# Performance work log

Measured on AMD Instinct MI355X. Metric: run time of the kernel, lower is better.

Reference implementation:

```python
import jax, jax.numpy as jnp
import numpy as np
import math

HIDDEN = 1024
NUM_HEADS = 16
HEAD_DIM = HIDDEN // NUM_HEADS
B, S = 4, 1024


def setup_inputs() -> dict:
    key = jax.random.key(0)
    ks = jax.random.split(key, 16)
    sd = 1.0 / math.sqrt(HIDDEN)
    inp = {
        "x": jax.random.normal(ks[0], (B, S, HIDDEN), jnp.float32),
        "spikes": jax.random.uniform(ks[1], (B, S, HIDDEN), jnp.float32),
        "membrane_potential": jax.random.normal(ks[2], (B, S, HIDDEN), jnp.float32),
        "Wq": jax.random.normal(ks[3], (HIDDEN, HIDDEN), jnp.float32) * sd,
        "bq": jnp.zeros((HIDDEN,), jnp.float32),
        "Wk": jax.random.normal(ks[4], (HIDDEN, HIDDEN), jnp.float32) * sd,
        "bk": jnp.zeros((HIDDEN,), jnp.float32),
        "Wv": jax.random.normal(ks[5], (HIDDEN, HIDDEN), jnp.float32) * sd,
        "bv": jnp.zeros((HIDDEN,), jnp.float32),
        "Wo": jax.random.normal(ks[6], (HIDDEN, HIDDEN), jnp.float32) * sd,
        "bo": jnp.zeros((HIDDEN,), jnp.float32),
        "tau_decay": jnp.ones((NUM_HEADS,), jnp.float32) * 10.0,
        "Wg": jax.random.normal(ks[7], (HIDDEN, 2 * HIDDEN), jnp.float32) * sd,
        "bg": jnp.zeros((HIDDEN,), jnp.float32),
    }
    return inp


def _heads(t):  # [B,S,H] -> [B,nH,S,hd]
    Bv, Sv, _ = t.shape
    return t.reshape(Bv, Sv, NUM_HEADS, HEAD_DIM).transpose(0, 2, 1, 3)


def reference(x, spikes, membrane_potential, Wq, bq, Wk, bk, Wv, bv, Wo, bo, tau_decay, Wg, bg):
    scale = 1.0 / math.sqrt(HEAD_DIM)
    q = _heads(x @ Wq.T + bq)
    k = _heads(x @ Wk.T + bk)
    v = _heads(x @ Wv.T + bv)

    # raw scores [B,nH,S,S]
    scores = jnp.einsum('bhqd,bhkd->bhqk', q, k) * scale

    # per-head exponential temporal decay mask [nH,S,S]
    times = jnp.arange(S, dtype=jnp.float32)
    tdiff = jnp.abs(times[:, None] - times[None, :])  # [S,S]
    tmask = jnp.exp(-tdiff[None] / tau_decay[:, None, None])
    scores = scores * tmask[None]

    # spike correlation term
    sm = _heads(spikes)
    spike_attn = jnp.einsum('bhqd,bhkd->bhqk', sm, sm) * scale
    scores = scores * (1.0 + spike_attn)

    # membrane gating of V
    v = v * jax.nn.sigmoid(_heads(membrane_potential))

    probs = jax.nn.softmax(scores, axis=-1)
    context = jnp.einsum('bhqk,bhkd->bhqd', probs, v)
    context = context.transpose(0, 2, 1, 3).reshape(B, S, HIDDEN)

    # dendritic gate
    gate_in = jnp.concatenate([context, membrane_potential], axis=-1)
    gate = jax.nn.sigmoid(gate_in @ Wg.T + bg)
    context = context * gate

    return context @ Wo.T + bo
```

## Files before the change

### kernel.cpp

```cpp
#include <hip/hip_runtime.h>
#include <math.h>
#include <stdint.h>

namespace {

typedef __attribute__((ext_vector_type(8))) short s8v;
typedef __attribute__((ext_vector_type(4))) float f4v;
typedef unsigned short u16;

__device__ __forceinline__ float fexp2(float x) {
  return __builtin_amdgcn_exp2f(x);
}

__device__ __forceinline__ u16 f2bf(float f) {
  union { float f; uint32_t u; } v; v.f = f;
  uint32_t r = v.u + 0x7fffu + ((v.u >> 16) & 1u);
  return (u16)(r >> 16);
}
__device__ __forceinline__ float bf2f(u16 h) {
  union { uint32_t u; float f; } v; v.u = ((uint32_t)h) << 16;
  return v.f;
}
__device__ __forceinline__ uint32_t pk2r(float a, float b) {
  return (uint32_t)f2bf(a) | ((uint32_t)f2bf(b) << 16);
}
__device__ __forceinline__ uint32_t pk2(float a, float b) {
  union { float f; uint32_t u; } x, y; x.f = a; y.f = b;
  return ((x.u + 0x8000u) >> 16) | ((y.u + 0x8000u) & 0xffff0000u);
}
__device__ __forceinline__ float sigmoidf_(float x) { return 1.0f / (1.0f + __expf(-x)); }

__device__ __forceinline__ void gload16(const u16* g, u16* l) {
  __builtin_amdgcn_global_load_lds(
      (const __attribute__((address_space(1))) void*)g,
      (__attribute__((address_space(3))) void*)l, 16, 0, 0);
}

struct CvtJob { const float* src; u16* dst; };
struct CvtArgs { CvtJob j[18]; float* vz; };

__global__ __launch_bounds__(256) void cvt_kernel(CvtArgs a) {
  if (blockIdx.y == 0 && blockIdx.x < 4) {
    float4 z; z.x = 0.f; z.y = 0.f; z.z = 0.f; z.w = 0.f;
    ((float4*)a.vz)[blockIdx.x * 256 + threadIdx.x] = z;
  }
  const CvtJob jb = a.j[blockIdx.y];
  const int i = blockIdx.x * 256 + threadIdx.x;
  const float4 v = ((const float4*)jb.src)[i];
  uint2 pk;
  pk.x = pk2r(v.x, v.y);
  pk.y = pk2r(v.z, v.w);
  ((uint2*)jb.dst)[i] = pk;
}

__global__ __launch_bounds__(768, 3) void qkv_gemm(
    const u16* __restrict__ xb,
    const u16* __restrict__ Wqb, const u16* __restrict__ Wkb, const u16* __restrict__ Wvb,
    const float* __restrict__ bq, const float* __restrict__ bk, const float* __restrict__ bv,
    const u16* __restrict__ memb,
    u16* __restrict__ Qb, u16* __restrict__ Kb, u16* __restrict__ Vt,
    float* __restrict__ Vtot) {
  __shared__ __align__(16) u16 as_[4][4096];
  __shared__ __align__(16) u16 bs_[4][12288];
  const int t = threadIdx.x;
  const int nb = blockIdx.x, mb = blockIdx.y;
  const int m0 = mb * 128, n0 = nb * 128;
  const int l = t & 63, w = t >> 6;
  const int mat = w >> 2;
  const int wl = w & 3, wm = wl >> 1, wn = wl & 1;
  const int lr = l & 15, lq = l >> 4;
  const int rh = lr >> 1;
  const int rb4 = (lr & 1) << 2;
  const int bmat = mat * 4096;

  const f4v fz = {0.f, 0.f, 0.f, 0.f};
  f4v acc[4][4];
#pragma unroll
  for (int i = 0; i < 4; ++i)
#pragma unroll
    for (int j = 0; j < 4; ++j) acc[i][j] = fz;

  const int tt = t & 255, uu = (t >> 8) & 1;
  const int sc0 = (tt & 7) ^ ((tt >> 3) & 7);
  const int sgrow = ((tt >> 3) << 1) + (sc0 >> 2);
  const int sgk = (sc0 & 3) << 3;
  const bool stg = (t < 512);

  const u16* ga = xb + (size_t)(m0 + uu * 64 + sgrow) * 1024 + sgk;
  const u16* gq = Wqb + (size_t)(n0 + uu * 64 + sgrow) * 1024 + sgk;
  const u16* gk = Wkb + (size_t)(n0 + uu * 64 + sgrow) * 1024 + sgk;
  const u16* gv = Wvb + (size_t)(n0 + uu * 64 + sgrow) * 1024 + sgk;
  const int lofs = uu * 2048 + tt * 8;

#define QKV_STAGE(c)                                                           \
  {                                                                            \
    const int ko_ = (c) * 32;                                                  \
    const int bb_ = (c) & 3;                                                   \
    gload16(ga + ko_, &as_[bb_][lofs]);                                        \
    gload16(gq + ko_, &bs_[bb_][lofs]);                                        \
    gload16(gk + ko_, &bs_[bb_][4096 + lofs]);                                 \
    gload16(gv + ko_, &bs_[bb_][8192 + lofs]);                                 \
  }

  if (stg) { QKV_STAGE(0); QKV_STAGE(1); QKV_STAGE(2); }
  asm volatile("s_waitcnt vmcnt(8)" ::: "memory");
  __builtin_amdgcn_s_barrier();

  const int co = ((rb4 + lq) ^ rh) * 8;
  for (int c = 0; c < 32; ++c) {
    const int cb = c & 3;
    const bool st = (c + 3 < 32);
    s8v af[4], bf[4];
#pragma unroll
    for (int mi = 0; mi < 4; ++mi)
      af[mi] = *(const s8v*)(&as_[cb][(wm * 32 + mi * 8 + rh) * 64 + co]);
#pragma unroll
    for (int ni = 0; ni < 4; ++ni)
      bf[ni] = *(const s8v*)(&bs_[cb][bmat + (wn * 32 + ni * 8 + rh) * 64 + co]);
    if (stg && st) QKV_STAGE(c + 3);
    __builtin_amdgcn_s_barrier();
    asm volatile("s_waitcnt lgkmcnt(0)" ::: "memory");
    __builtin_amdgcn_sched_barrier(0);
    __builtin_amdgcn_s_setprio(1);
    if (mat < 2) {
#pragma unroll
      for (int mi = 0; mi < 4; ++mi)
#pragma unroll
        for (int ni = 0; ni < 4; ++ni)
          acc[mi][ni] = __builtin_amdgcn_mfma_f32_16x16x32_bf16(
              bf[ni], af[mi], acc[mi][ni], 0, 0, 0);
    } else {
#pragma unroll
      for (int mi = 0; mi < 4; ++mi)
#pragma unroll
        for (int ni = 0; ni < 4; ++ni)
          acc[mi][ni] = __builtin_amdgcn_mfma_f32_16x16x32_bf16(
              af[mi], bf[ni], acc[mi][ni], 0, 0, 0);
    }
    __builtin_amdgcn_s_setprio(0);
    if (st) {
      asm volatile("s_waitcnt vmcnt(8)" ::: "memory");
    } else if (c == 29) {
      asm volatile("s_waitcnt vmcnt(4)" ::: "memory");
    } else if (c == 30) {
      asm volatile("s_waitcnt vmcnt(0)" ::: "memory");
    }
    if (c < 31) __builtin_amdgcn_s_barrier();
  }
#undef QKV_STAGE
  __builtin_amdgcn_sched_barrier(0);

  if (mat < 2) {
    u16* dst = (mat == 0) ? Qb : Kb;
    const float* bias = (mat == 0) ? bq : bk;
#pragma unroll
    for (int mi = 0; mi < 4; ++mi)
#pragma unroll
      for (int ni = 0; ni < 4; ++ni) {
        const int m = m0 + wm * 64 + mi * 16 + lr;
        const int nb4 = n0 + wn * 64 + ni * 16 + lq * 4;
        const float4 b4 = *(const float4*)&bias[nb4];
        uint2 pk;
        pk.x = pk2r(acc[mi][ni][0] + b4.x, acc[mi][ni][1] + b4.y);
        pk.y = pk2r(acc[mi][ni][2] + b4.z, acc[mi][ni][3] + b4.w);
        *(uint2*)(dst + (size_t)m * 1024 + nb4) = pk;
      }
  } else {
    const int b = m0 >> 10;
    float vpart[4] = {0.f, 0.f, 0.f, 0.f};
#pragma unroll
    for (int mi = 0; mi < 4; ++mi)
#pragma unroll
      for (int ni = 0; ni < 4; ++ni) {
        const int mrow = m0 + wm * 64 + mi * 16 + lq * 4;
        const int ncol = n0 + wn * 64 + ni * 16 + lr;
        const int h = ncol >> 6, d = ncol & 63;
        const float bi = bv[ncol];
        float tv[4];
#pragma unroll
        for (int r = 0; r < 4; ++r)
          tv[r] = (acc[mi][ni][r] + bi) *
                  sigmoidf_(bf2f(memb[(size_t)(mrow + r) * 1024 + ncol]));
        vpart[ni] += (tv[0] + tv[1]) + (tv[2] + tv[3]);
        const int s = mrow & 1023;
        uint2 pk;
        pk.x = pk2r(tv[0], tv[1]);
        pk.y = pk2r(tv[2], tv[3]);
        *(uint2*)(Vt + ((size_t)((b * 16 + h) * 64 + d)) * 1024 + s) = pk;
      }
#pragma unroll
    for (int ni = 0; ni < 4; ++ni) {
      const int ncol = n0 + wn * 64 + ni * 16 + lr;
      atomicAdd(&Vtot[(size_t)(b * 16 + (ncol >> 6)) * 64 + (ncol & 63)], vpart[ni]);
    }
  }
}

template <int MODE>
__global__ __launch_bounds__(512, 2) void gemm64(
    const u16* __restrict__ Ab, const u16* __restrict__ A2b,
    const u16* __restrict__ W, const float* __restrict__ bias,
    u16* __restrict__ outb, float* __restrict__ outf, int K) {
  __shared__ __align__(16) u16 as_[4][4096], bs_[4][4096];
  const int t = threadIdx.x;
  const int m0 = blockIdx.y * 128, n0 = blockIdx.x * 128;
  const int l = t & 63, w = t >> 6;
  const int wm = w >> 2, wn = w & 3;
  const int lr = l & 15, lq = l >> 4;
  const int rh = lr >> 1, rb4 = (lr & 1) << 2;
  const f4v fz = {0.f, 0.f, 0.f, 0.f};
  f4v acc[4][2];
#pragma unroll
  for (int i = 0; i < 4; ++i)
#pragma unroll
    for (int j = 0; j < 2; ++j) acc[i][j] = fz;

  const int tt = t & 255, uu = t >> 8;
  const int sc0 = (tt & 7) ^ ((tt >> 3) & 7);
  const int sgrow = ((tt >> 3) << 1) + (sc0 >> 2);
  const int sgk = (sc0 & 3) << 3;
  const u16* ga1 = Ab + (size_t)(m0 + uu * 64 + sgrow) * 1024 + sgk;
  const u16* ga2 = (MODE == 1)
      ? (A2b + (size_t)(m0 + uu * 64 + sgrow) * 1024 + sgk) : ga1;
  const u16* gw = W + (size_t)(n0 + uu * 64 + sgrow) * K + sgk;
  const int lofs = uu * 2048 + tt * 8;
  const int nc = K >> 5;

#define G_STAGE_A(c)                                                           \
  {                                                                            \
    const int ko_ = (c) * 32;                                                  \
    if (MODE == 1 && ko_ >= 1024) gload16(ga2 + (ko_ - 1024), &as_[(c) & 3][lofs]); \
    else gload16(ga1 + ko_, &as_[(c) & 3][lofs]);                              \
  }
#define G_STAGE_W(c) gload16(gw + (c) * 32, &bs_[(c) & 3][lofs])

  G_STAGE_A(0); G_STAGE_W(0);
  G_STAGE_A(1); G_STAGE_W(1);
  G_STAGE_A(2); G_STAGE_W(2);
  asm volatile("s_waitcnt vmcnt(4)" ::: "memory");
  __builtin_amdgcn_s_barrier();

  const int co = ((rb4 + lq) ^ rh) * 8;
  for (int c = 0; c < nc; ++c) {
    const int cb = c & 3;
    s8v af[4], bf[2];
#pragma unroll
    for (int mi = 0; mi < 4; ++mi)
      af[mi] = *(const s8v*)(&as_[cb][(wm * 32 + mi * 8 + rh) * 64 + co]);
#pragma unroll
    for (int ni = 0; ni < 2; ++ni)
      bf[ni] = *(const s8v*)(&bs_[cb][(wn * 16 + ni * 8 + rh) * 64 + co]);
    if (c + 3 < nc) { G_STAGE_A(c + 3); G_STAGE_W(c + 3); }
    __builtin_amdgcn_s_barrier();
    asm volatile("s_waitcnt lgkmcnt(0)" ::: "memory");
    __builtin_amdgcn_sched_barrier(0);
    __builtin_amdgcn_s_setprio(1);
#pragma unroll
    for (int mi = 0; mi < 4; ++mi)
#pragma unroll
      for (int ni = 0; ni < 2; ++ni)
        acc[mi][ni] = __builtin_amdgcn_mfma_f32_16x16x32_bf16(
            bf[ni], af[mi], acc[mi][ni], 0, 0, 0);
    __builtin_amdgcn_s_setprio(0);
    if (c + 3 < nc) {
      asm volatile("s_waitcnt vmcnt(4)" ::: "memory");
    } else if (c + 3 == nc) {
      asm volatile("s_waitcnt vmcnt(2)" ::: "memory");
    } else if (c + 2 == nc) {
      asm volatile("s_waitcnt vmcnt(0)" ::: "memory");
    }
    if (c + 1 < nc) __builtin_amdgcn_s_barrier();
  }
#undef G_STAGE_A
#undef G_STAGE_W
  __builtin_amdgcn_sched_barrier(0);

#pragma unroll
  for (int mi = 0; mi < 4; ++mi)
#pragma unroll
    for (int ni = 0; ni < 2; ++ni) {
      const int m = m0 + wm * 64 + mi * 16 + lr;
      const int nb4 = n0 + wn * 32 + ni * 16 + lq * 4;
      const float4 b4 = *(const float4*)&bias[nb4];
      if (MODE == 0) {
        float4 o;
        o.x = acc[mi][ni][0] + b4.x; o.y = acc[mi][ni][1] + b4.y;
        o.z = acc[mi][ni][2] + b4.z; o.w = acc[mi][ni][3] + b4.w;
        *(float4*)(outf + (size_t)m * 1024 + nb4) = o;
      } else {
        const uint2 a2 = *(const uint2*)(Ab + (size_t)m * 1024 + nb4);
        float cx[4] = {bf2f((u16)(a2.x & 0xffff)), bf2f((u16)(a2.x >> 16)),
                       bf2f((u16)(a2.y & 0xffff)), bf2f((u16)(a2.y >> 16))};
        float g[4];
        g[0] = cx[0] * sigmoidf_(acc[mi][ni][0] + b4.x);
        g[1] = cx[1] * sigmoidf_(acc[mi][ni][1] + b4.y);
        g[2] = cx[2] * sigmoidf_(acc[mi][ni][2] + b4.z);
        g[3] = cx[3] * sigmoidf_(acc[mi][ni][3] + b4.w);
        uint2 pk;
        pk.x = pk2r(g[0], g[1]);
        pk.y = pk2r(g[2], g[3]);
        *(uint2*)(outb + (size_t)m * 1024 + nb4) = pk;
      }
    }
}

__global__ __launch_bounds__(256) void attn_mfma(
    const u16* __restrict__ Qb, const u16* __restrict__ Kb,
    const u16* __restrict__ SPb, const u16* __restrict__ Vt,
    const float* __restrict__ tau, const float* __restrict__ Vtot,
    u16* __restrict__ CTXb) {
  __shared__ u16 kbuf[4096], skbuf[4096], vbuf[4096];
  __shared__ u16 pbuf[4][16 * 64];
  const int t = threadIdx.x, l = t & 63, w = t >> 6;
  const int lr = l & 15, lq = l >> 4;
  const int p = blockIdx.x;
  const int g = (p & 7) + 8 * (p >> 7);
  const int qt = (p >> 3) & 15;
  const int h = g & 15, b = g >> 4;

  const float tv_ = tau[h];
  const float c2 = 1.44269504088896f / tv_;
  const float K0 = 0.125f * 1.44269504088896f;
  int rad = (int)ceilf(tv_ * 0.171875f);
  if (rad > 15) rad = 15;
  const int jlo = (qt - rad < 0) ? 0 : qt - rad;
  const int jhi = (qt + rad > 15) ? 15 : qt + rad;
  const int farCnt = 16 - (jhi - jlo + 1);

  float cN[4], cNi[4], cR[4], cRi[4];
#pragma unroll
  for (int i = 0; i < 4; ++i) {
    cN[i]  = fexp2(c2 * (float)(i * 16));
    cNi[i] = fexp2(-c2 * (float)(i * 16));
    cR[i]  = fexp2(c2 * (float)(lq * 4 + i));
    cRi[i] = fexp2(-c2 * (float)(lq * 4 + i));
  }

  s8v qf[2], sf[2];
  {
    const size_t base = ((size_t)(b * 1024 + qt * 64 + w * 16 + lr)) * 1024 + h * 64 + lq * 8;
    qf[0] = *(const s8v*)(Qb + base);
    qf[1] = *(const s8v*)(Qb + base + 32);
    sf[0] = *(const s8v*)(SPb + base);
    sf[1] = *(const s8v*)(SPb + base + 32);
  }
  const s8v ones = {0x3F80, 0x3F80, 0x3F80, 0x3F80, 0x3F80, 0x3F80, 0x3F80, 0x3F80};

  const f4v fz = {0.f, 0.f, 0.f, 0.f};
  f4v oacc[4], vs[4];
  float lacc[4];
#pragma unroll
  for (int i = 0; i < 4; ++i) { oacc[i] = fz; vs[i] = fz; lacc[i] = 0.f; }

  const int iqw = qt * 64 + w * 16;
  const int srow = t >> 3;
  const int csw = ((t & 7) ^ (srow & 7)) * 8;
  const int rx = lr & 7;
  u16* pw = pbuf[w];

  for (int jc = jlo; jc <= jhi; ++jc) {
    const int j0 = jc * 64;
    __syncthreads();
    {
      const size_t kg = ((size_t)(b * 1024 + j0 + srow)) * 1024 + h * 64 + csw;
      gload16(Kb + kg, kbuf + t * 8);
      gload16(Kb + kg + 32 * 1024, kbuf + 2048 + t * 8);
      gload16(SPb + kg, skbuf + t * 8);
      gload16(SPb + kg + 32 * 1024, skbuf + 2048 + t * 8);
      const size_t vg = ((size_t)((b * 16 + h) * 64 + srow)) * 1024 + j0 + csw;
      gload16(Vt + vg, vbuf + t * 8);
      gload16(Vt + vg + 32 * 1024, vbuf + 2048 + t * 8);
    }
    __syncthreads();

    f4v sa[4], ssa[4];
#pragma unroll
    for (int ni = 0; ni < 4; ++ni) { sa[ni] = fz; ssa[ni] = fz; }
#pragma unroll
    for (int ks = 0; ks < 2; ++ks) {
#pragma unroll
      for (int ni = 0; ni < 4; ++ni) {
        const int off = (ni * 16 + lr) * 64 + (((ks * 4 + lq) ^ rx) * 8);
        const s8v kf = *(const s8v*)(kbuf + off);
        sa[ni] = __builtin_amdgcn_mfma_f32_16x16x32_bf16(kf, qf[ks], sa[ni], 0, 0, 0);
        const s8v skf = *(const s8v*)(skbuf + off);
        ssa[ni] = __builtin_amdgcn_mfma_f32_16x16x32_bf16(skf, sf[ks], ssa[ni], 0, 0, 0);
      }
    }

    const int D0 = iqw - j0;
    float pv[4][4];
    if (jc < qt) {
      const float EA = K0 * fexp2(-c2 * (float)(D0 + lr));
#pragma unroll
      for (int ni = 0; ni < 4; ++ni)
#pragma unroll
        for (int r = 0; r < 4; ++r) {
          const float t1 = fmaf(ssa[ni][r], 0.125f, 1.0f);
          const float e = fexp2(sa[ni][r] * cN[ni] * cR[r] * EA * t1);
          pv[ni][r] = e;
          lacc[ni] += e;
        }
    } else if (jc > qt) {
      const float EAi = K0 * fexp2(c2 * (float)(D0 + lr));
#pragma unroll
      for (int ni = 0; ni < 4; ++ni)
#pragma unroll
        for (int r = 0; r < 4; ++r) {
          const float t1 = fmaf(ssa[ni][r], 0.125f, 1.0f);
          const float e = fexp2(sa[ni][r] * cNi[ni] * cRi[r] * EAi * t1);
          pv[ni][r] = e;
          lacc[ni] += e;
        }
    } else {
      const float EA  = K0 * fexp2(-c2 * (float)(D0 + lr));
      const float EAi = K0 * fexp2(c2 * (float)(D0 + lr));
#pragma unroll
      for (int ni = 0; ni < 4; ++ni)
#pragma unroll
        for (int r = 0; r < 4; ++r) {
          const int jloc = ni * 16 + lq * 4 + r;
          const float fb = cN[ni] * cR[r] * EA;
          const float fa = cNi[ni] * cRi[r] * EAi;
          const float f = (D0 + lr >= jloc) ? fb : fa;
          const float t1 = fmaf(ssa[ni][r], 0.125f, 1.0f);
          const float e = fexp2(sa[ni][r] * f * t1);
          pv[ni][r] = e;
          lacc[ni] += e;
        }
    }

#pragma unroll
    for (int ni = 0; ni < 4; ++ni) {
      const int phys = (ni * 2 + (lq >> 1)) ^ rx;
      uint2 p2;
      p2.x = pk2(pv[ni][0], pv[ni][1]);
      p2.y = pk2(pv[ni][2], pv[ni][3]);
      *(uint2*)(pw + lr * 64 + phys * 8 + (lq & 1) * 4) = p2;
    }

#pragma unroll
    for (int ks = 0; ks < 2; ++ks) {
      const s8v pf = *(const s8v*)(pw + lr * 64 + (((ks * 4 + lq) ^ rx) * 8));
#pragma unroll
      for (int nd = 0; nd < 4; ++nd) {
        const int off = (nd * 16 + lr) * 64 + (((ks * 4 + lq) ^ rx) * 8);
        const s8v vf = *(const s8v*)(vbuf + off);
        oacc[nd] = __builtin_amdgcn_mfma_f32_16x16x32_bf16(vf, pf, oacc[nd], 0, 0, 0);
        vs[nd] = __builtin_amdgcn_mfma_f32_16x16x32_bf16(vf, ones, vs[nd], 0, 0, 0);
      }
    }
  }

  float ls = (lacc[0] + lacc[1]) + (lacc[2] + lacc[3]);
  ls += __shfl_xor(ls, 16);
  ls += __shfl_xor(ls, 32);
  ls += 64.0f * (float)farCnt;
  const float inv = 1.0f / ls;
  const float* vt0 = Vtot + (size_t)(b * 16 + h) * 64;
  const size_t orow = ((size_t)(b * 1024 + qt * 64 + w * 16 + lr)) * 1024 + h * 64;
#pragma unroll
  for (int nd = 0; nd < 4; ++nd) {
    const float4 vt4 = *(const float4*)(vt0 + nd * 16 + lq * 4);
    float o0 = (oacc[nd][0] + vt4.x - vs[nd][0]) * inv;
    float o1 = (oacc[nd][1] + vt4.y - vs[nd][1]) * inv;
    float o2 = (oacc[nd][2] + vt4.z - vs[nd][2]) * inv;
    float o3 = (oacc[nd][3] + vt4.w - vs[nd][3]) * inv;
    uint2 o;
    o.x = pk2r(o0, o1);
    o.y = pk2r(o2, o3);
    *(uint2*)(CTXb + orow + nd * 16 + lq * 4) = o;
  }
}

}

extern "C" void kernel_launch(void* const* d_in, const int* in_sizes, int n_in,
                              void* d_out, int out_size, void* d_ws, size_t ws_size,
                              hipStream_t stream) {
  const float* x      = (const float*)d_in[0];
  const float* spikes = (const float*)d_in[1];
  const float* mem    = (const float*)d_in[2];
  const float* Wq     = (const float*)d_in[3];
  const float* bq     = (const float*)d_in[4];
  const float* Wk     = (const float*)d_in[5];
  const float* bk     = (const float*)d_in[6];
  const float* Wv     = (const float*)d_in[7];
  const float* bv     = (const float*)d_in[8];
  const float* Wo     = (const float*)d_in[9];
  const float* bo     = (const float*)d_in[10];
  const float* tau    = (const float*)d_in[11];
  const float* Wg     = (const float*)d_in[12];
  const float* bg     = (const float*)d_in[13];
  float* out = (float*)d_out;

  uint8_t* w8 = (uint8_t*)d_ws;
  u16* spb  = (u16*)(w8);
  u16* xb   = (u16*)(w8 + (8u << 20));
  u16* Wqb  = (u16*)(w8 + (16u << 20));
  u16* Wkb  = (u16*)(w8 + (18u << 20));
  u16* Wvb  = (u16*)(w8 + (20u << 20));
  u16* Wob  = (u16*)(w8 + (22u << 20));
  u16* Wgb  = (u16*)(w8 + (24u << 20));
  u16* Qb   = (u16*)(w8 + (28u << 20));
  u16* Kb   = (u16*)(w8 + (36u << 20));
  u16* Vt   = (u16*)(w8 + (44u << 20));
  u16* CTXb = (u16*)(w8 + (52u << 20));
  float* Vtot = (float*)(w8 + (60u << 20));
  u16* memb = (u16*)d_out;
  u16* gctx = xb;

  constexpr size_t QE = 262144 * 4;
  CvtArgs ca;
  for (int q = 0; q < 4; ++q) ca.j[q]     = {x + q * QE,      xb + q * QE};
  for (int q = 0; q < 4; ++q) ca.j[4 + q] = {spikes + q * QE, spb + q * QE};
  for (int q = 0; q < 4; ++q) ca.j[8 + q] = {mem + q * QE,    memb + q * QE};
  ca.j[12] = {Wq, Wqb};
  ca.j[13] = {Wk, Wkb};
  ca.j[14] = {Wv, Wvb};
  ca.j[15] = {Wo, Wob};
  ca.j[16] = {Wg, Wgb};
  ca.j[17] = {Wg + QE, Wgb + QE};
  ca.vz = Vtot;
  cvt_kernel<<<dim3(1024, 18), 256, 0, stream>>>(ca);

  qkv_gemm<<<dim3(8, 32), 768, 0, stream>>>(xb, Wqb, Wkb, Wvb, bq, bk, bv, memb,
                                            Qb, Kb, Vt, Vtot);
  attn_mfma<<<dim3(1024), 256, 0, stream>>>(Qb, Kb, spb, Vt, tau, Vtot, CTXb);
  gemm64<1><<<dim3(8, 32), 512, 0, stream>>>(CTXb, memb, Wgb, bg, gctx, nullptr, 2048);
  gemm64<0><<<dim3(8, 32), 512, 0, stream>>>(gctx, nullptr, Wob, bo, nullptr, out, 1024);
}
```

Before: 254.2 us.

## Halve QKV GEMM N-tile to 64, use 384-thread blocks and double buffering

The fused QKV projection kernel now computes a 128x64 tile per matrix with 6 waves (2 per Q/K/V) instead of 128x128 with 12 waves. The grid doubles to 512 blocks, and LDS staging drops from a 4-deep to a 2-deep ring with reworked load assignments. The goal is better CU fill and lower LDS use per block. In exchange, each block reuses the A tile less and has a shallower prefetch pipeline.

After: 250.3 us. No clear change (-1.5%).

```diff
diff --git a/kernel.cpp b/kernel.cpp
--- a/kernel.cpp
+++ b/kernel.cpp
@@ -53,25 +53,25 @@
   ((uint2*)jb.dst)[i] = pk;
 }
 
-__global__ __launch_bounds__(768, 3) void qkv_gemm(
+__global__ __launch_bounds__(384, 3) void qkv_gemm(
     const u16* __restrict__ xb,
     const u16* __restrict__ Wqb, const u16* __restrict__ Wkb, const u16* __restrict__ Wvb,
     const float* __restrict__ bq, const float* __restrict__ bk, const float* __restrict__ bv,
     const u16* __restrict__ memb,
     u16* __restrict__ Qb, u16* __restrict__ Kb, u16* __restrict__ Vt,
     float* __restrict__ Vtot) {
-  __shared__ __align__(16) u16 as_[4][4096];
-  __shared__ __align__(16) u16 bs_[4][12288];
+  __shared__ __align__(16) u16 as_[2][4096];
+  __shared__ __align__(16) u16 bs_[2][6144];
   const int t = threadIdx.x;
   const int nb = blockIdx.x, mb = blockIdx.y;
-  const int m0 = mb * 128, n0 = nb * 128;
+  const int m0 = mb * 128, n0 = nb * 64;
   const int l = t & 63, w = t >> 6;
-  const int mat = w >> 2;
-  const int wl = w & 3, wm = wl >> 1, wn = wl & 1;
+  const int mat = w >> 1;
+  const int wm = w & 1;
   const int lr = l & 15, lq = l >> 4;
   const int rh = lr >> 1;
   const int rb4 = (lr & 1) << 2;
-  const int bmat = mat * 4096;
+  const int bmat = mat * 2048;
 
   const f4v fz = {0.f, 0.f, 0.f, 0.f};
   f4v acc[4][4];
@@ -80,47 +80,58 @@
 #pragma unroll
     for (int j = 0; j < 4; ++j) acc[i][j] = fz;
 
-  const int tt = t & 255, uu = (t >> 8) & 1;
-  const int sc0 = (tt & 7) ^ ((tt >> 3) & 7);
-  const int sgrow = ((tt >> 3) << 1) + (sc0 >> 2);
-  const int sgk = (sc0 & 3) << 3;
-  const bool stg = (t < 512);
-
-  const u16* ga = xb + (size_t)(m0 + uu * 64 + sgrow) * 1024 + sgk;
-  const u16* gq = Wqb + (size_t)(n0 + uu * 64 + sgrow) * 1024 + sgk;
-  const u16* gk = Wkb + (size_t)(n0 + uu * 64 + sgrow) * 1024 + sgk;
-  const u16* gv = Wvb + (size_t)(n0 + uu * 64 + sgrow) * 1024 + sgk;
-  const int lofs = uu * 2048 + tt * 8;
+  const int sc0a = (t & 7) ^ ((t >> 3) & 7);
+  const int sgrowa = (((t & 255) >> 3) << 1) + (sc0a >> 2);
+  const int sgka = (sc0a & 3) << 3;
+  const u16* ga0 = xb + (size_t)(m0 + sgrowa) * 1024 + sgka;
+  const u16* ga1 = xb + (size_t)(m0 + 64 + sgrowa) * 1024 + sgka;
+  const int tq1 = t & 255;
+  const int tq2 = (t < 128) ? (t + 128) : (t - 128);
+  const u16* wb1 = (t < 256) ? Wqb : Wkb;
+  const u16* wb2 = (t < 128) ? Wkb : Wvb;
+  const int sc01 = (tq1 & 7) ^ ((tq1 >> 3) & 7);
+  const int sc02 = (tq2 & 7) ^ ((tq2 >> 3) & 7);
+  const u16* gb1 = wb1 + (size_t)(n0 + ((tq1 >> 3) << 1) + (sc01 >> 2)) * 1024 +
+                   ((sc01 & 3) << 3);
+  const u16* gb2 = wb2 + (size_t)(n0 + ((tq2 >> 3) << 1) + (sc02 >> 2)) * 1024 +
+                   ((sc02 & 3) << 3);
+  const int mb1 = ((t < 256) ? 0 : 2048) + tq1 * 8;
+  const int mb2 = ((t < 128) ? 2048 : 4096) + tq2 * 8;
 
 #define QKV_STAGE(c)                                                           \
   {                                                                            \
     const int ko_ = (c) * 32;                                                  \
-    const int bb_ = (c) & 3;                                                   \
-    gload16(ga + ko_, &as_[bb_][lofs]);                                        \
-    gload16(gq + ko_, &bs_[bb_][lofs]);                                        \
-    gload16(gk + ko_, &bs_[bb_][4096 + lofs]);                                 \
-    gload16(gv + ko_, &bs_[bb_][8192 + lofs]);                                 \
-  }
-
-  if (stg) { QKV_STAGE(0); QKV_STAGE(1); QKV_STAGE(2); }
-  asm volatile("s_waitcnt vmcnt(8)" ::: "memory");
+    const int bb_ = (c) & 1;                                                   \
+    if (t < 256) {                                                             \
+      gload16(ga0 + ko_, &as_[bb_][(t & 255) * 8]);                            \
+      gload16(ga1 + ko_, &as_[bb_][2048 + (t & 255) * 8]);                     \
+    }                                                                          \
+    gload16(gb1 + ko_, &bs_[bb_][mb1]);                                        \
+    gload16(gb2 + ko_, &bs_[bb_][mb2]);                                        \
+  }
+
+  QKV_STAGE(0); QKV_STAGE(1);
+  if (w < 4) {
+    asm volatile("s_waitcnt vmcnt(4)" ::: "memory");
+  } else {
+    asm volatile("s_waitcnt vmcnt(2)" ::: "memory");
+  }
   __builtin_amdgcn_s_barrier();
 
   const int co = ((rb4 + lq) ^ rh) * 8;
   for (int c = 0; c < 32; ++c) {
-    const int cb = c & 3;
-    const bool st = (c + 3 < 32);
+    const int cb = c & 1;
     s8v af[4], bf[4];
 #pragma unroll
     for (int mi = 0; mi < 4; ++mi)
       af[mi] = *(const s8v*)(&as_[cb][(wm * 32 + mi * 8 + rh) * 64 + co]);
 #pragma unroll
     for (int ni = 0; ni < 4; ++ni)
-      bf[ni] = *(const s8v*)(&bs_[cb][bmat + (wn * 32 + ni * 8 + rh) * 64 + co]);
-    if (stg && st) QKV_STAGE(c + 3);
-    __builtin_amdgcn_s_barrier();
+      bf[ni] = *(const s8v*)(&bs_[cb][bmat + (ni * 8 + rh) * 64 + co]);
     asm volatile("s_waitcnt lgkmcnt(0)" ::: "memory");
     __builtin_amdgcn_sched_barrier(0);
+    __builtin_amdgcn_s_barrier();
+    if (c + 2 < 32) QKV_STAGE(c + 2);
     __builtin_amdgcn_s_setprio(1);
     if (mat < 2) {
 #pragma unroll
@@ -138,10 +149,12 @@
               af[mi], bf[ni], acc[mi][ni], 0, 0, 0);
     }
     __builtin_amdgcn_s_setprio(0);
-    if (st) {
-      asm volatile("s_waitcnt vmcnt(8)" ::: "memory");
-    } else if (c == 29) {
-      asm volatile("s_waitcnt vmcnt(4)" ::: "memory");
+    if (c + 2 < 32) {
+      if (w < 4) {
+        asm volatile("s_waitcnt vmcnt(4)" ::: "memory");
+      } else {
+        asm volatile("s_waitcnt vmcnt(2)" ::: "memory");
+      }
     } else if (c == 30) {
       asm volatile("s_waitcnt vmcnt(0)" ::: "memory");
     }
@@ -158,7 +171,7 @@
 #pragma unroll
       for (int ni = 0; ni < 4; ++ni) {
         const int m = m0 + wm * 64 + mi * 16 + lr;
-        const int nb4 = n0 + wn * 64 + ni * 16 + lq * 4;
+        const int nb4 = n0 + ni * 16 + lq * 4;
         const float4 b4 = *(const float4*)&bias[nb4];
         uint2 pk;
         pk.x = pk2r(acc[mi][ni][0] + b4.x, acc[mi][ni][1] + b4.y);
@@ -173,7 +186,7 @@
 #pragma unroll
       for (int ni = 0; ni < 4; ++ni) {
         const int mrow = m0 + wm * 64 + mi * 16 + lq * 4;
-        const int ncol = n0 + wn * 64 + ni * 16 + lr;
+        const int ncol = n0 + ni * 16 + lr;
         const int h = ncol >> 6, d = ncol & 63;
         const float bi = bv[ncol];
         float tv[4];
@@ -190,7 +203,7 @@
       }
 #pragma unroll
     for (int ni = 0; ni < 4; ++ni) {
-      const int ncol = n0 + wn * 64 + ni * 16 + lr;
+      const int ncol = n0 + ni * 16 + lr;
       atomicAdd(&Vtot[(size_t)(b * 16 + (ncol >> 6)) * 64 + (ncol & 63)], vpart[ni]);
     }
   }
@@ -524,8 +537,8 @@
   ca.vz = Vtot;
   cvt_kernel<<<dim3(1024, 18), 256, 0, stream>>>(ca);
 
-  qkv_gemm<<<dim3(8, 32), 768, 0, stream>>>(xb, Wqb, Wkb, Wvb, bq, bk, bv, memb,
-                                            Qb, Kb, Vt, Vtot);
+  qkv_gemm<<<dim3(16, 32), 384, 0, stream>>>(xb, Wqb, Wkb, Wvb, bq, bk, bv, memb,
+                                             Qb, Kb, Vt, Vtot);
   attn_mfma<<<dim3(1024), 256, 0, stream>>>(Qb, Kb, spb, Vt, tau, Vtot, CTXb);
   gemm64<1><<<dim3(8, 32), 512, 0, stream>>>(CTXb, memb, Wgb, bg, gctx, nullptr, 2048);
   gemm64<0><<<dim3(8, 32), 512, 0, stream>>>(gctx, nullptr, Wob, bo, nullptr, out, 1024);
```
